# Performance work log

Hardware: AMD Instinct MI355X
Metric: run time of the kernel (lower is better)

The kernel has to match this reference:

```python
import jax, jax.numpy as jnp
import numpy as np

N_NODES = 100000
N_EDGES = 3200000
D_FEAT = 128
N1 = 128
N2 = 64
NUM_CLASSES = 10
NUM_GRAPHS = 256


def gcn_conv(x, edge_index, W, b, num_nodes):
    """PyG GCNConv: y = D^-1/2 (A+I) D^-1/2 (x W) + b, self-loops added."""
    src, dst = edge_index[0], edge_index[1]
    # degree including self-loop (edge weight 1)
    deg = jax.ops.segment_sum(jnp.ones_like(dst, dtype=x.dtype), dst,
                              num_segments=num_nodes) + 1.0
    dis = jnp.where(deg > 0, deg ** -0.5, 0.0)  # deg_inv_sqrt, [N]
    h = x @ W                                    # transform first, [N, out]
    norm = dis[src] * dis[dst]                   # [E]
    msg = h[src] * norm[:, None]                 # gather + scale, [E, out]
    agg = jax.ops.segment_sum(msg, dst, num_segments=num_nodes)
    agg = agg + h * (dis * dis)[:, None]         # self-loop contribution
    return agg + b


def global_mean_pool(x, batch, num_graphs):
    sums = jax.ops.segment_sum(x, batch, num_segments=num_graphs)
    cnt = jax.ops.segment_sum(jnp.ones((x.shape[0],), dtype=x.dtype), batch,
                              num_segments=num_graphs)
    return sums / jnp.maximum(cnt, 1.0)[:, None]


def setup_inputs() -> dict:
    key = jax.random.key(0)
    ks = jax.random.split(key, 8)
    x = jax.random.normal(ks[0], (N_NODES, D_FEAT), dtype=jnp.float32)
    edge_index = jax.random.randint(ks[1], (2, N_EDGES), 0, N_NODES, dtype=jnp.int64)
    batch = jnp.sort(jax.random.randint(ks[2], (N_NODES,), 0, NUM_GRAPHS, dtype=jnp.int64))
    W1 = jax.random.normal(ks[3], (D_FEAT, N1), dtype=jnp.float32) / np.sqrt(D_FEAT)
    b1 = jnp.zeros((N1,), dtype=jnp.float32)
    W2 = jax.random.normal(ks[4], (N1, N2), dtype=jnp.float32) / np.sqrt(N1)
    b2 = jnp.zeros((N2,), dtype=jnp.float32)
    Wfc = jax.random.normal(ks[5], (N2, NUM_CLASSES), dtype=jnp.float32) / np.sqrt(N2)
    bfc = jnp.zeros((NUM_CLASSES,), dtype=jnp.float32)
    return {"x": x, "edge_index": edge_index, "batch": batch,
            "W1": W1, "b1": b1, "W2": W2, "b2": b2,
            "Wfc": Wfc, "bfc": bfc, "num_graphs": NUM_GRAPHS}


def reference(x, edge_index, batch, W1, b1, W2, b2, Wfc, bfc, num_graphs):
    n = x.shape[0]
    h = gcn_conv(x, edge_index, W1, b1, n)
    h = jax.nn.relu(h)
    h = gcn_conv(h, edge_index, W2, b2, n)
    g = global_mean_pool(h, batch, num_graphs)   # [num_graphs, N2]
    # dropout is identity at inference
    return g @ Wfc + bfc                          # [num_graphs, num_classes]
```

## Files before the change

kernel.cpp:

```cpp
#include <hip/hip_runtime.h>
#include <math.h>

typedef unsigned int  u32;
typedef unsigned short u16;

#define TILE1 8192
#define BKW   256
#define CAP   9216

typedef __attribute__((ext_vector_type(8))) short bf16x8;
typedef __attribute__((ext_vector_type(4))) float f32x4;
typedef __attribute__((ext_vector_type(2))) float f32x2;
union frag_u { bf16x8 v; u32 u[4]; uint4 q; };

__device__ inline u32 bf16_rne(float f) {
    u32 u = __float_as_uint(f);
    return (u + 0x7FFFu + ((u >> 16) & 1u)) >> 16;
}
__device__ inline float bf_lo(u32 u) { return __uint_as_float(u << 16); }
__device__ inline float bf_hi(u32 u) { return __uint_as_float(u & 0xFFFF0000u); }

__device__ inline f32x2 up2(u32 u) {
    f32x2 t;
    t.x = __uint_as_float(u << 16);
    t.y = __uint_as_float(u & 0xFFFF0000u);
    return t;
}
__device__ inline void add8p(f32x2* a, uint4 q) {
    a[0] += up2(q.x); a[1] += up2(q.y); a[2] += up2(q.z); a[3] += up2(q.w);
}

__device__ inline u32 relu_pk(u32 v) {
    u32 s = v & 0x80008000u;
    u32 m = (s >> 15) * 0xFFFFu;
    return v & ~m;
}


__global__ __launch_bounds__(512) void k_part1(const int* __restrict__ ei,
                                               int* __restrict__ bucketCur,
                                               u32* __restrict__ tmp,
                                               int E, int N, int NBK) {
    __shared__ int hist[1024];
    __shared__ int base[512];
    const int tid = threadIdx.x;
    if (tid < NBK) { hist[tid] = 0; hist[512 + tid] = 0; }
    __syncthreads();

    const int rep = (tid & 1) << 9;
    const int t0 = blockIdx.x * TILE1;
    const int4* ei4s = (const int4*)ei;
    const int4* ei4d = (const int4*)(ei + E);
    const int q0 = t0 >> 2;
    const int QE = E >> 2;

    int sv[16], dv[16], key[16];
#pragma unroll
    for (int j = 0; j < 4; ++j) {
        int qi = q0 + j * 512 + tid;
        int4 s4 = make_int4(0, 0, 0, 0), d4 = make_int4(-1, -1, -1, -1);
        if (qi < QE) { s4 = ei4s[qi]; d4 = ei4d[qi]; }
        sv[4 * j + 0] = s4.x; dv[4 * j + 0] = d4.x;
        sv[4 * j + 1] = s4.y; dv[4 * j + 1] = d4.y;
        sv[4 * j + 2] = s4.z; dv[4 * j + 2] = d4.z;
        sv[4 * j + 3] = s4.w; dv[4 * j + 3] = d4.w;
    }
#pragma unroll
    for (int j = 0; j < 16; ++j) {
        key[j] = -1;
        if ((unsigned)dv[j] < (unsigned)N && (unsigned)sv[j] < (unsigned)N) {
            key[j] = dv[j] >> 8;
            atomicAdd(&hist[key[j] + rep], 1);
        }
    }
    __syncthreads();
    if (tid < NBK) {
        int tot = hist[tid] + hist[512 + tid];
        base[tid] = atomicAdd(&bucketCur[tid], tot);
        hist[tid] = 0;
    }
    __syncthreads();
#pragma unroll
    for (int j = 0; j < 16; ++j) {
        if (key[j] >= 0) {
            int slot = atomicAdd(&hist[key[j]], 1);
            int off = base[key[j]] + slot;
            if (off < CAP)
                tmp[(size_t)key[j] * CAP + off] =
                    ((u32)(dv[j] & 255) << 17) | (u32)sv[j];
        }
    }
}

__global__ __launch_bounds__(512) void k_part2(const int* __restrict__ bucketCnt,
                                               const u32* __restrict__ tmp,
                                               int* __restrict__ csr,
                                               int* __restrict__ rowptr,
                                               float* __restrict__ dis,
                                               int* __restrict__ gdegH,
                                               int N, int NBK) {
    __shared__ int hist[256];
    __shared__ int ts[512];
    __shared__ int degh[256];
    __shared__ int sStart;
    const int b = blockIdx.x;
    const int t = threadIdx.x;

    if (t < 256) degh[t] = 0;
    int myCnt = (t < NBK) ? bucketCnt[t] : 0;
    ts[t] = myCnt;
    __syncthreads();
    for (int off = 1; off < 512; off <<= 1) {
        int u = (t >= off) ? ts[t - off] : 0;
        __syncthreads();
        ts[t] += u;
        __syncthreads();
    }
    if (t == b) sStart = ts[t] - myCnt;
    if (b == 0 && t == NBK - 1) rowptr[N] = ts[t];
    __syncthreads();
    const int start = sStart;
    const int cnt = bucketCnt[b];
    const u32* src = tmp + (size_t)b * CAP;

    if (t < 256) hist[t] = 0;
    __syncthreads();
    for (int i = t; i < cnt; i += 512)
        atomicAdd(&hist[src[i] >> 17], 1);
    __syncthreads();

    int h = (t < 256) ? hist[t] : 0;
    ts[t] = h;
    __syncthreads();
    for (int off = 1; off < 512; off <<= 1) {
        int u = (t >= off) ? ts[t - off] : 0;
        __syncthreads();
        ts[t] += u;
        __syncthreads();
    }
    if (t < 256) hist[t] = ts[t] - h;
    __syncthreads();

    if (t < 256) {
        int gn = (b << 8) + t;
        if (gn < N) {
            int e0 = hist[t];
            int e1 = (t < 255) ? hist[t + 1] : cnt;
            rowptr[gn] = start + e0;
            int d = e1 - e0;
            dis[gn] = rsqrtf((float)d + 1.0f);
            atomicAdd(&degh[d < 255 ? d : 255], 1);
        }
    }
    __syncthreads();

    if (t < 256 && degh[t]) atomicAdd(&gdegH[t], degh[t]);

    for (int i = t; i < cnt; i += 512) {
        u32 v = src[i];
        int p = atomicAdd(&hist[v >> 17], 1);
        csr[start + p] = (int)(v & 0x1FFFFu);
    }
}


__global__ __launch_bounds__(256) void k_prefix(const int* __restrict__ gdegH,
                                                int* __restrict__ binBase) {
    __shared__ int ts[256];
    int t = threadIdx.x;
    int v = gdegH[t];
    ts[t] = v;
    __syncthreads();
    for (int off = 1; off < 256; off <<= 1) {
        int u = (t >= off) ? ts[t - off] : 0;
        __syncthreads();
        ts[t] += u;
        __syncthreads();
    }
    binBase[t] = ts[t] - v;
}

__global__ __launch_bounds__(512) void k_scatter(const int* __restrict__ rowptr,
                                                 int* __restrict__ binBase,
                                                 int* __restrict__ perm, int N) {
    __shared__ int lh[256];
    __shared__ int lb[256];
    int t = threadIdx.x;
    int i = blockIdx.x * 512 + t;
    if (t < 256) lh[t] = 0;
    __syncthreads();
    int d = 0, slot = 0;
    if (i < N) {
        d = rowptr[i + 1] - rowptr[i];
        if (d > 255) d = 255;
        slot = atomicAdd(&lh[d], 1);
    }
    __syncthreads();
    if (t < 256) lb[t] = lh[t] ? atomicAdd(&binBase[t], lh[t]) : 0;
    __syncthreads();
    if (i < N) perm[lb[d] + slot] = i;
}


__global__ __launch_bounds__(256) void k_convW(
    const float* __restrict__ W1, const float* __restrict__ W2,
    u32* __restrict__ W1h, u32* __restrict__ W1l,
    u32* __restrict__ W2h, u32* __restrict__ W2l,
    int* __restrict__ bucketCur, int* __restrict__ gdegH, int NBK)
{
    int idx = blockIdx.x * 256 + threadIdx.x;
    if (idx < NBK) bucketCur[idx] = 0;
    if (idx < 256) gdegH[idx] = 0;
    if (idx < 8192) {
        int n = idx >> 6, k = (idx & 63) * 2;
        float w0 = W1[k * 128 + n], w1 = W1[(k + 1) * 128 + n];
        u32 h0 = bf16_rne(w0), h1 = bf16_rne(w1);
        u32 l0 = bf16_rne(w0 - __uint_as_float(h0 << 16));
        u32 l1 = bf16_rne(w1 - __uint_as_float(h1 << 16));
        W1h[idx] = h0 | (h1 << 16);
        W1l[idx] = l0 | (l1 << 16);
    } else if (idx < 12288) {
        int i2 = idx - 8192;
        int n = i2 >> 6, k = (i2 & 63) * 2;
        float w0 = W2[k * 64 + n], w1 = W2[(k + 1) * 64 + n];
        u32 h0 = bf16_rne(w0), h1 = bf16_rne(w1);
        u32 l0 = bf16_rne(w0 - __uint_as_float(h0 << 16));
        u32 l1 = bf16_rne(w1 - __uint_as_float(h1 << 16));
        W2h[i2] = h0 | (h1 << 16);
        W2l[i2] = l0 | (l1 << 16);
    }
}


__global__ __launch_bounds__(256) void k_gemm1m(
    const float* __restrict__ X, const u32* __restrict__ Wh,
    const u32* __restrict__ Wl, const float* __restrict__ dis,
    u32* __restrict__ Hb, int M)
{
    __shared__ uint4 sW[4096];
    const int tid = threadIdx.x;
    const uint4* Wh4 = (const uint4*)Wh;
    const uint4* Wl4 = (const uint4*)Wl;
#pragma unroll
    for (int i = 0; i < 8; ++i) {
        int idx = tid + i * 256;
        int l = idx >> 4, j = idx & 15;
        int js = j ^ (l & 7);
        sW[l * 16 + js] = Wh4[idx];
        sW[2048 + l * 16 + js] = Wl4[idx];
    }
    __syncthreads();

    const int w = tid >> 6, lane = tid & 63;
    const int mrow = blockIdx.x * 64 + w * 16;
    const int m16 = lane & 15, quad = lane >> 4;
    int gm = mrow + m16; if (gm >= M) gm = M - 1;

    frag_u Ah[4], Al[4];
    const float* xr = X + (size_t)gm * 128;
#pragma unroll
    for (int kt = 0; kt < 4; ++kt) {
        int kb = kt * 32 + quad * 8;
        float4 xa = *(const float4*)(xr + kb);
        float4 xb = *(const float4*)(xr + kb + 4);
        float xe[8] = {xa.x, xa.y, xa.z, xa.w, xb.x, xb.y, xb.z, xb.w};
#pragma unroll
        for (int j = 0; j < 4; ++j) {
            u32 h0 = bf16_rne(xe[2 * j]),     h1 = bf16_rne(xe[2 * j + 1]);
            u32 l0 = bf16_rne(xe[2 * j]     - __uint_as_float(h0 << 16));
            u32 l1 = bf16_rne(xe[2 * j + 1] - __uint_as_float(h1 << 16));
            Ah[kt].u[j] = h0 | (h1 << 16);
            Al[kt].u[j] = l0 | (l1 << 16);
        }
    }

    float dv[4];
#pragma unroll
    for (int r = 0; r < 4; ++r) {
        int gR = mrow + quad * 4 + r;
        dv[r] = (gR < M) ? dis[gR] : 0.f;
    }

#pragma unroll
    for (int nt = 0; nt < 8; ++nt) {
        f32x4 acc = {0.f, 0.f, 0.f, 0.f};
        int l = nt * 16 + m16;
        int swz = l & 7;
#pragma unroll
        for (int kt = 0; kt < 4; ++kt) {
            frag_u Bh, Bl;
            int jb = (kt * 4 + quad) ^ swz;
            Bh.q = sW[l * 16 + jb];
            Bl.q = sW[2048 + l * 16 + jb];
            acc = __builtin_amdgcn_mfma_f32_16x16x32_bf16(Al[kt].v, Bh.v, acc, 0, 0, 0);
            acc = __builtin_amdgcn_mfma_f32_16x16x32_bf16(Ah[kt].v, Bl.v, acc, 0, 0, 0);
            acc = __builtin_amdgcn_mfma_f32_16x16x32_bf16(Ah[kt].v, Bh.v, acc, 0, 0, 0);
        }
#pragma unroll
        for (int r = 0; r < 4; ++r) {
            float vs = acc[r] * dv[r];
            float vo = __shfl_xor(vs, 1, 64);
            if ((m16 & 1) == 0) {
                int gR = mrow + quad * 4 + r;
                if (gR < M)
                    Hb[(size_t)gR * 64 + nt * 8 + (m16 >> 1)] =
                        bf16_rne(vs) | (bf16_rne(vo) << 16);
            }
        }
    }
}


__global__ __launch_bounds__(256) void k_gemm2m(
    const u32* __restrict__ Xb, const u32* __restrict__ Wh,
    const u32* __restrict__ Wl, const float* __restrict__ dis,
    u32* __restrict__ Hb, int M)
{
    __shared__ uint4 sW[2176];
    const int tid = threadIdx.x;
    const uint4* Wh4 = (const uint4*)Wh;
    const uint4* Wl4 = (const uint4*)Wl;
#pragma unroll
    for (int i = 0; i < 4; ++i) {
        int idx = tid + i * 256;
        int l = idx >> 4, j = idx & 15;
        sW[l * 17 + j] = Wh4[l * 16 + j];
        sW[1088 + l * 17 + j] = Wl4[l * 16 + j];
    }
    __syncthreads();

    const int w = tid >> 6, lane = tid & 63;
    const int mrow = blockIdx.x * 64 + w * 16;
    const int m16 = lane & 15, quad = lane >> 4;
    int gm = mrow + m16; if (gm >= M) gm = M - 1;

    const uint4* X4 = (const uint4*)Xb;
    frag_u A[4];
#pragma unroll
    for (int kt = 0; kt < 4; ++kt) {
        A[kt].q = X4[(size_t)gm * 16 + kt * 4 + quad];
#pragma unroll
        for (int j = 0; j < 4; ++j) A[kt].u[j] = relu_pk(A[kt].u[j]);
    }

    float dv[4];
#pragma unroll
    for (int r = 0; r < 4; ++r) {
        int gR = mrow + quad * 4 + r;
        dv[r] = (gR < M) ? dis[gR] : 0.f;
    }

#pragma unroll
    for (int nt = 0; nt < 4; ++nt) {
        f32x4 acc = {0.f, 0.f, 0.f, 0.f};
        int l = nt * 16 + m16;
#pragma unroll
        for (int kt = 0; kt < 4; ++kt) {
            frag_u Bh, Bl;
            Bh.q = sW[l * 17 + kt * 4 + quad];
            Bl.q = sW[1088 + l * 17 + kt * 4 + quad];
            acc = __builtin_amdgcn_mfma_f32_16x16x32_bf16(A[kt].v, Bl.v, acc, 0, 0, 0);
            acc = __builtin_amdgcn_mfma_f32_16x16x32_bf16(A[kt].v, Bh.v, acc, 0, 0, 0);
        }
#pragma unroll
        for (int r = 0; r < 4; ++r) {
            float vs = acc[r] * dv[r];
            float vo = __shfl_xor(vs, 1, 64);
            if ((m16 & 1) == 0) {
                int gR = mrow + quad * 4 + r;
                if (gR < M)
                    Hb[(size_t)gR * 32 + nt * 8 + (m16 >> 1)] =
                        bf16_rne(vs) | (bf16_rne(vo) << 16);
            }
        }
    }
}


template <int LGS>
__global__ __launch_bounds__(256) void k_aggs(
    const int* __restrict__ rowptr, const int* __restrict__ csr,
    const int* __restrict__ perm, const float* __restrict__ dis,
    const u32* __restrict__ Hb, const float* __restrict__ bias,
    u32* __restrict__ AGGb, int N)
{
    const int LG = 1 << LGS;
    const int SH = LGS + 4;
    int gid = blockIdx.x * 256 + threadIdx.x;
    int s = gid >> LGS;
    int li = threadIdx.x & (LG - 1);
    if (s >= N) return;
    int n = perm[s];
    int e = rowptr[n];
    int s1 = rowptr[n + 1];
    const float dn = dis[n];
    const char* hb = (const char*)Hb;
    const u32 off = (u32)li << 4;

    f32x2 acc[4];
#pragma unroll
    for (int j = 0; j < 4; ++j) acc[j] = 0.f;

    for (; e + 8 <= s1; e += 8) {
        u32 b0 = (u32)csr[e + 0] << SH;
        u32 b1 = (u32)csr[e + 1] << SH;
        u32 b2 = (u32)csr[e + 2] << SH;
        u32 b3 = (u32)csr[e + 3] << SH;
        u32 b4 = (u32)csr[e + 4] << SH;
        u32 b5 = (u32)csr[e + 5] << SH;
        u32 b6 = (u32)csr[e + 6] << SH;
        u32 b7 = (u32)csr[e + 7] << SH;
        uint4 q0 = *(const uint4*)(hb + b0 + off);
        uint4 q1 = *(const uint4*)(hb + b1 + off);
        uint4 q2 = *(const uint4*)(hb + b2 + off);
        uint4 q3 = *(const uint4*)(hb + b3 + off);
        uint4 q4 = *(const uint4*)(hb + b4 + off);
        uint4 q5 = *(const uint4*)(hb + b5 + off);
        uint4 q6 = *(const uint4*)(hb + b6 + off);
        uint4 q7 = *(const uint4*)(hb + b7 + off);
        add8p(acc, q0); add8p(acc, q1); add8p(acc, q2); add8p(acc, q3);
        add8p(acc, q4); add8p(acc, q5); add8p(acc, q6); add8p(acc, q7);
    }
    for (; e + 2 <= s1; e += 2) {
        u32 b0 = (u32)csr[e + 0] << SH;
        u32 b1 = (u32)csr[e + 1] << SH;
        uint4 q0 = *(const uint4*)(hb + b0 + off);
        uint4 q1 = *(const uint4*)(hb + b1 + off);
        add8p(acc, q0); add8p(acc, q1);
    }
    if (e < s1) {
        u32 b0 = (u32)csr[e] << SH;
        uint4 q0 = *(const uint4*)(hb + b0 + off);
        add8p(acc, q0);
    }
    {
        uint4 q = *(const uint4*)(hb + ((u32)n << SH) + off);
        add8p(acc, q);
    }

    float4 b0 = ((const float4*)bias)[li * 2 + 0];
    float4 b1 = ((const float4*)bias)[li * 2 + 1];
    uint4 p;
    p.x = bf16_rne(fmaf(dn, acc[0].x, b0.x)) | (bf16_rne(fmaf(dn, acc[0].y, b0.y)) << 16);
    p.y = bf16_rne(fmaf(dn, acc[1].x, b0.z)) | (bf16_rne(fmaf(dn, acc[1].y, b0.w)) << 16);
    p.z = bf16_rne(fmaf(dn, acc[2].x, b1.x)) | (bf16_rne(fmaf(dn, acc[2].y, b1.y)) << 16);
    p.w = bf16_rne(fmaf(dn, acc[3].x, b1.z)) | (bf16_rne(fmaf(dn, acc[3].y, b1.w)) << 16);
    ((uint4*)AGGb)[(size_t)n * LG + li] = p;
}


__device__ inline int lower_bound(const int* __restrict__ b, int n, int v) {
    int lo = 0, hi = n;
    while (lo < hi) { int m = (lo + hi) >> 1; if (b[m] < v) lo = m + 1; else hi = m; }
    return lo;
}

__global__ __launch_bounds__(256) void k_poolfc(
    const int* __restrict__ batch, const u32* __restrict__ AGGb2,
    const float* __restrict__ Wfc, const float* __restrict__ bfc,
    float* __restrict__ out, int n)
{
    int g = blockIdx.x;
    int start = lower_bound(batch, n, g);
    int end   = lower_bound(batch, n, g + 1);
    int tid = threadIdx.x;
    int f = tid & 63, stripe = tid >> 6;
    int ui = f >> 1, hi = f & 1;
    float acc = 0.f;
    for (int i = start + stripe; i < end; i += 4) {
        u32 v = AGGb2[(size_t)i * 32 + ui];
        acc += hi ? bf_hi(v) : bf_lo(v);
    }
    __shared__ float red[256];
    __shared__ float mean[64];
    red[tid] = acc;
    __syncthreads();
    if (tid < 64) {
        float s = red[tid] + red[tid + 64] + red[tid + 128] + red[tid + 192];
        float c = (float)(end - start);
        mean[tid] = s / fmaxf(c, 1.0f);
    }
    __syncthreads();
    if (tid < 10) {
        float o = bfc[tid];
        for (int k = 0; k < 64; ++k)
            o = fmaf(mean[k], Wfc[k * 10 + tid], o);
        out[g * 10 + tid] = o;
    }
}


extern "C" void kernel_launch(void* const* d_in, const int* in_sizes, int n_in,
                              void* d_out, int out_size, void* d_ws, size_t ws_size,
                              hipStream_t stream)
{
    const float* x    = (const float*)d_in[0];
    const int*   ei   = (const int*)d_in[1];
    const int*   batch= (const int*)d_in[2];
    const float* W1   = (const float*)d_in[3];
    const float* b1   = (const float*)d_in[4];
    const float* W2   = (const float*)d_in[5];
    const float* b2   = (const float*)d_in[6];
    const float* Wfc  = (const float*)d_in[7];
    const float* bfc  = (const float*)d_in[8];
    float* out = (float*)d_out;

    const int N  = in_sizes[0] / 128;
    const int E  = in_sizes[1] / 2;
    const int ng = out_size / 10;

    const int NBK = (N + BKW - 1) / BKW;

    int*   rowptr    = (int*)d_ws;
    int*   bucketCur = rowptr + 102400;
    float* dis       = (float*)(bucketCur + 512);
    int*   csr       = (int*)(dis + 102400);
    u32*   tmp       = (u32*)(csr + E);
    u32*   Hb1       = tmp;
    u32*   agg2b     = tmp;
    u32*   agg1b     = (u32*)((int*)tmp + (size_t)N * 64);
    u16*   Hb2       = (u16*)((int*)agg1b + (size_t)N * 128);
    u32*   W1h       = (u32*)((int*)Hb2 + (size_t)N * 32);
    u32*   W1l       = W1h + 8192;
    u32*   W2h       = W1l + 8192;
    u32*   W2l       = W2h + 4096;
    int*   perm      = (int*)(W2l + 4096);
    int*   gdegH     = perm + N;
    int*   binBase   = gdegH + 256;

    k_convW<<<48, 256, 0, stream>>>(W1, W2, W1h, W1l, W2h, W2l, bucketCur, gdegH, NBK);
    k_part1<<<(E + TILE1 - 1) / TILE1, 512, 0, stream>>>(ei, bucketCur, tmp, E, N, NBK);
    k_part2<<<NBK, 512, 0, stream>>>(bucketCur, tmp, csr, rowptr, dis, gdegH, N, NBK);
    k_prefix<<<1, 256, 0, stream>>>(gdegH, binBase);
    k_scatter<<<(N + 511) / 512, 512, 0, stream>>>(rowptr, binBase, perm, N);

    k_gemm1m<<<(N + 63) / 64, 256, 0, stream>>>(x, W1h, W1l, dis, Hb1, N);
    k_aggs<4><<<(N * 16 + 255) / 256, 256, 0, stream>>>(rowptr, csr, perm, dis, Hb1, b1, agg1b, N);

    k_gemm2m<<<(N + 63) / 64, 256, 0, stream>>>(agg1b, W2h, W2l, dis, (u32*)Hb2, N);
    k_aggs<3><<<(N * 8 + 255) / 256, 256, 0, stream>>>(rowptr, csr, perm, dis, (const u32*)Hb2, b2, agg2b, N);

    k_poolfc<<<ng, 256, 0, stream>>>(batch, agg2b, Wfc, bfc, out, N);
}
```

Measured before the change: 404.4 us.

## Drop degree-sorted permutation, split layer-1 aggregation into column halves, widen GEMM tiles

Removes the degree histogram, prefix and scatter kernels that built a degree-sorted node permutation, so the aggregation now walks nodes in natural order. The 128-wide layer-1 aggregation runs as two passes over 64-column halves, each with 8 lanes per node, which shrinks the gathered working set per pass and may improve cache hit rates at the cost of reading the CSR twice. Both GEMM kernels now compute 32 rows per wave (128 per block), reusing each B fragment loaded from shared memory across two MFMA tiles. The risks are load imbalance without degree sorting and higher register pressure in the GEMMs.

```diff
diff --git a/kernel.cpp b/kernel.cpp
--- a/kernel.cpp
+++ b/kernel.cpp
@@ -97,16 +97,13 @@
                                                int* __restrict__ csr,
                                                int* __restrict__ rowptr,
                                                float* __restrict__ dis,
-                                               int* __restrict__ gdegH,
                                                int N, int NBK) {
     __shared__ int hist[256];
     __shared__ int ts[512];
-    __shared__ int degh[256];
     __shared__ int sStart;
     const int b = blockIdx.x;
     const int t = threadIdx.x;
 
-    if (t < 256) degh[t] = 0;
     int myCnt = (t < NBK) ? bucketCnt[t] : 0;
     ts[t] = myCnt;
     __syncthreads();
@@ -147,14 +144,10 @@
             int e0 = hist[t];
             int e1 = (t < 255) ? hist[t + 1] : cnt;
             rowptr[gn] = start + e0;
-            int d = e1 - e0;
-            dis[gn] = rsqrtf((float)d + 1.0f);
-            atomicAdd(&degh[d < 255 ? d : 255], 1);
-        }
-    }
-    __syncthreads();
-
-    if (t < 256 && degh[t]) atomicAdd(&gdegH[t], degh[t]);
+            dis[gn] = rsqrtf((float)(e1 - e0) + 1.0f);
+        }
+    }
+    __syncthreads();
 
     for (int i = t; i < cnt; i += 512) {
         u32 v = src[i];
@@ -164,53 +157,14 @@
 }
 
 
-__global__ __launch_bounds__(256) void k_prefix(const int* __restrict__ gdegH,
-                                                int* __restrict__ binBase) {
-    __shared__ int ts[256];
-    int t = threadIdx.x;
-    int v = gdegH[t];
-    ts[t] = v;
-    __syncthreads();
-    for (int off = 1; off < 256; off <<= 1) {
-        int u = (t >= off) ? ts[t - off] : 0;
-        __syncthreads();
-        ts[t] += u;
-        __syncthreads();
-    }
-    binBase[t] = ts[t] - v;
-}
-
-__global__ __launch_bounds__(512) void k_scatter(const int* __restrict__ rowptr,
-                                                 int* __restrict__ binBase,
-                                                 int* __restrict__ perm, int N) {
-    __shared__ int lh[256];
-    __shared__ int lb[256];
-    int t = threadIdx.x;
-    int i = blockIdx.x * 512 + t;
-    if (t < 256) lh[t] = 0;
-    __syncthreads();
-    int d = 0, slot = 0;
-    if (i < N) {
-        d = rowptr[i + 1] - rowptr[i];
-        if (d > 255) d = 255;
-        slot = atomicAdd(&lh[d], 1);
-    }
-    __syncthreads();
-    if (t < 256) lb[t] = lh[t] ? atomicAdd(&binBase[t], lh[t]) : 0;
-    __syncthreads();
-    if (i < N) perm[lb[d] + slot] = i;
-}
-
-
 __global__ __launch_bounds__(256) void k_convW(
     const float* __restrict__ W1, const float* __restrict__ W2,
     u32* __restrict__ W1h, u32* __restrict__ W1l,
     u32* __restrict__ W2h, u32* __restrict__ W2l,
-    int* __restrict__ bucketCur, int* __restrict__ gdegH, int NBK)
+    int* __restrict__ bucketCur, int NBK)
 {
     int idx = blockIdx.x * 256 + threadIdx.x;
     if (idx < NBK) bucketCur[idx] = 0;
-    if (idx < 256) gdegH[idx] = 0;
     if (idx < 8192) {
         int n = idx >> 6, k = (idx & 63) * 2;
         float w0 = W1[k * 128 + n], w1 = W1[(k + 1) * 128 + n];
@@ -252,38 +206,44 @@
     __syncthreads();
 
     const int w = tid >> 6, lane = tid & 63;
-    const int mrow = blockIdx.x * 64 + w * 16;
+    const int mrow = blockIdx.x * 128 + w * 32;
     const int m16 = lane & 15, quad = lane >> 4;
-    int gm = mrow + m16; if (gm >= M) gm = M - 1;
-
-    frag_u Ah[4], Al[4];
-    const float* xr = X + (size_t)gm * 128;
-#pragma unroll
-    for (int kt = 0; kt < 4; ++kt) {
-        int kb = kt * 32 + quad * 8;
-        float4 xa = *(const float4*)(xr + kb);
-        float4 xb = *(const float4*)(xr + kb + 4);
-        float xe[8] = {xa.x, xa.y, xa.z, xa.w, xb.x, xb.y, xb.z, xb.w};
-#pragma unroll
-        for (int j = 0; j < 4; ++j) {
-            u32 h0 = bf16_rne(xe[2 * j]),     h1 = bf16_rne(xe[2 * j + 1]);
-            u32 l0 = bf16_rne(xe[2 * j]     - __uint_as_float(h0 << 16));
-            u32 l1 = bf16_rne(xe[2 * j + 1] - __uint_as_float(h1 << 16));
-            Ah[kt].u[j] = h0 | (h1 << 16);
-            Al[kt].u[j] = l0 | (l1 << 16);
-        }
-    }
-
-    float dv[4];
-#pragma unroll
-    for (int r = 0; r < 4; ++r) {
-        int gR = mrow + quad * 4 + r;
-        dv[r] = (gR < M) ? dis[gR] : 0.f;
-    }
+
+    frag_u Ah[2][4], Al[2][4];
+#pragma unroll
+    for (int t = 0; t < 2; ++t) {
+        int gm = mrow + t * 16 + m16; if (gm >= M) gm = M - 1;
+        const float* xr = X + (size_t)gm * 128;
+#pragma unroll
+        for (int kt = 0; kt < 4; ++kt) {
+            int kb = kt * 32 + quad * 8;
+            float4 xa = *(const float4*)(xr + kb);
+            float4 xb = *(const float4*)(xr + kb + 4);
+            float xe[8] = {xa.x, xa.y, xa.z, xa.w, xb.x, xb.y, xb.z, xb.w};
+#pragma unroll
+            for (int j = 0; j < 4; ++j) {
+                u32 h0 = bf16_rne(xe[2 * j]),     h1 = bf16_rne(xe[2 * j + 1]);
+                u32 l0 = bf16_rne(xe[2 * j]     - __uint_as_float(h0 << 16));
+                u32 l1 = bf16_rne(xe[2 * j + 1] - __uint_as_float(h1 << 16));
+                Ah[t][kt].u[j] = h0 | (h1 << 16);
+                Al[t][kt].u[j] = l0 | (l1 << 16);
+            }
+        }
+    }
+
+    float dv[2][4];
+#pragma unroll
+    for (int t = 0; t < 2; ++t)
+#pragma unroll
+        for (int r = 0; r < 4; ++r) {
+            int gR = mrow + t * 16 + quad * 4 + r;
+            dv[t][r] = (gR < M) ? dis[gR] : 0.f;
+        }
 
 #pragma unroll
     for (int nt = 0; nt < 8; ++nt) {
-        f32x4 acc = {0.f, 0.f, 0.f, 0.f};
+        f32x4 acc0 = {0.f, 0.f, 0.f, 0.f};
+        f32x4 acc1 = {0.f, 0.f, 0.f, 0.f};
         int l = nt * 16 + m16;
         int swz = l & 7;
 #pragma unroll
@@ -292,19 +252,28 @@
             int jb = (kt * 4 + quad) ^ swz;
             Bh.q = sW[l * 16 + jb];
             Bl.q = sW[2048 + l * 16 + jb];
-            acc = __builtin_amdgcn_mfma_f32_16x16x32_bf16(Al[kt].v, Bh.v, acc, 0, 0, 0);
-            acc = __builtin_amdgcn_mfma_f32_16x16x32_bf16(Ah[kt].v, Bl.v, acc, 0, 0, 0);
-            acc = __builtin_amdgcn_mfma_f32_16x16x32_bf16(Ah[kt].v, Bh.v, acc, 0, 0, 0);
+            acc0 = __builtin_amdgcn_mfma_f32_16x16x32_bf16(Al[0][kt].v, Bh.v, acc0, 0, 0, 0);
+            acc0 = __builtin_amdgcn_mfma_f32_16x16x32_bf16(Ah[0][kt].v, Bl.v, acc0, 0, 0, 0);
+            acc0 = __builtin_amdgcn_mfma_f32_16x16x32_bf16(Ah[0][kt].v, Bh.v, acc0, 0, 0, 0);
+            acc1 = __builtin_amdgcn_mfma_f32_16x16x32_bf16(Al[1][kt].v, Bh.v, acc1, 0, 0, 0);
+            acc1 = __builtin_amdgcn_mfma_f32_16x16x32_bf16(Ah[1][kt].v, Bl.v, acc1, 0, 0, 0);
+            acc1 = __builtin_amdgcn_mfma_f32_16x16x32_bf16(Ah[1][kt].v, Bh.v, acc1, 0, 0, 0);
         }
 #pragma unroll
         for (int r = 0; r < 4; ++r) {
-            float vs = acc[r] * dv[r];
-            float vo = __shfl_xor(vs, 1, 64);
+            float vs0 = acc0[r] * dv[0][r];
+            float vo0 = __shfl_xor(vs0, 1, 64);
+            float vs1 = acc1[r] * dv[1][r];
+            float vo1 = __shfl_xor(vs1, 1, 64);
             if ((m16 & 1) == 0) {
-                int gR = mrow + quad * 4 + r;
-                if (gR < M)
-                    Hb[(size_t)gR * 64 + nt * 8 + (m16 >> 1)] =
-                        bf16_rne(vs) | (bf16_rne(vo) << 16);
+                int gR0 = mrow + quad * 4 + r;
+                if (gR0 < M)
+                    Hb[(size_t)gR0 * 64 + nt * 8 + (m16 >> 1)] =
+                        bf16_rne(vs0) | (bf16_rne(vo0) << 16);
+                int gR1 = mrow + 16 + quad * 4 + r;
+                if (gR1 < M)
+                    Hb[(size_t)gR1 * 64 + nt * 8 + (m16 >> 1)] =
+                        bf16_rne(vs1) | (bf16_rne(vo1) << 16);
             }
         }
     }
@@ -330,72 +299,82 @@
     __syncthreads();
 
     const int w = tid >> 6, lane = tid & 63;
-    const int mrow = blockIdx.x * 64 + w * 16;
+    const int mrow = blockIdx.x * 128 + w * 32;
     const int m16 = lane & 15, quad = lane >> 4;
-    int gm = mrow + m16; if (gm >= M) gm = M - 1;
 
     const uint4* X4 = (const uint4*)Xb;
-    frag_u A[4];
-#pragma unroll
-    for (int kt = 0; kt < 4; ++kt) {
-        A[kt].q = X4[(size_t)gm * 16 + kt * 4 + quad];
-#pragma unroll
-        for (int j = 0; j < 4; ++j) A[kt].u[j] = relu_pk(A[kt].u[j]);
-    }
-
-    float dv[4];
-#pragma unroll
-    for (int r = 0; r < 4; ++r) {
-        int gR = mrow + quad * 4 + r;
-        dv[r] = (gR < M) ? dis[gR] : 0.f;
-    }
+    frag_u A[2][4];
+#pragma unroll
+    for (int t = 0; t < 2; ++t) {
+        int gm = mrow + t * 16 + m16; if (gm >= M) gm = M - 1;
+#pragma unroll
+        for (int kt = 0; kt < 4; ++kt) {
+            A[t][kt].q = X4[(size_t)gm * 16 + kt * 4 + quad];
+#pragma unroll
+            for (int j = 0; j < 4; ++j) A[t][kt].u[j] = relu_pk(A[t][kt].u[j]);
+        }
+    }
+
+    float dv[2][4];
+#pragma unroll
+    for (int t = 0; t < 2; ++t)
+#pragma unroll
+        for (int r = 0; r < 4; ++r) {
+            int gR = mrow + t * 16 + quad * 4 + r;
+            dv[t][r] = (gR < M) ? dis[gR] : 0.f;
+        }
 
 #pragma unroll
     for (int nt = 0; nt < 4; ++nt) {
-        f32x4 acc = {0.f, 0.f, 0.f, 0.f};
+        f32x4 acc0 = {0.f, 0.f, 0.f, 0.f};
+        f32x4 acc1 = {0.f, 0.f, 0.f, 0.f};
         int l = nt * 16 + m16;
 #pragma unroll
         for (int kt = 0; kt < 4; ++kt) {
             frag_u Bh, Bl;
             Bh.q = sW[l * 17 + kt * 4 + quad];
             Bl.q = sW[1088 + l * 17 + kt * 4 + quad];
-            acc = __builtin_amdgcn_mfma_f32_16x16x32_bf16(A[kt].v, Bl.v, acc, 0, 0, 0);
-            acc = __builtin_amdgcn_mfma_f32_16x16x32_bf16(A[kt].v, Bh.v, acc, 0, 0, 0);
+            acc0 = __builtin_amdgcn_mfma_f32_16x16x32_bf16(A[0][kt].v, Bl.v, acc0, 0, 0, 0);
+            acc0 = __builtin_amdgcn_mfma_f32_16x16x32_bf16(A[0][kt].v, Bh.v, acc0, 0, 0, 0);
+            acc1 = __builtin_amdgcn_mfma_f32_16x16x32_bf16(A[1][kt].v, Bl.v, acc1, 0, 0, 0);
+            acc1 = __builtin_amdgcn_mfma_f32_16x16x32_bf16(A[1][kt].v, Bh.v, acc1, 0, 0, 0);
         }
 #pragma unroll
         for (int r = 0; r < 4; ++r) {
-            float vs = acc[r] * dv[r];
-            float vo = __shfl_xor(vs, 1, 64);
+            float vs0 = acc0[r] * dv[0][r];
+            float vo0 = __shfl_xor(vs0, 1, 64);
+            float vs1 = acc1[r] * dv[1][r];
+            float vo1 = __shfl_xor(vs1, 1, 64);
             if ((m16 & 1) == 0) {
-                int gR = mrow + quad * 4 + r;
-                if (gR < M)
-                    Hb[(size_t)gR * 32 + nt * 8 + (m16 >> 1)] =
-                        bf16_rne(vs) | (bf16_rne(vo) << 16);
+                int gR0 = mrow + quad * 4 + r;
+                if (gR0 < M)
+                    Hb[(size_t)gR0 * 32 + nt * 8 + (m16 >> 1)] =
+                        bf16_rne(vs0) | (bf16_rne(vo0) << 16);
+                int gR1 = mrow + 16 + quad * 4 + r;
+                if (gR1 < M)
+                    Hb[(size_t)gR1 * 32 + nt * 8 + (m16 >> 1)] =
+                        bf16_rne(vs1) | (bf16_rne(vo1) << 16);
             }
         }
     }
 }
 
 
-template <int LGS>
-__global__ __launch_bounds__(256) void k_aggs(
+template <int SH, int POFF>
+__global__ __launch_bounds__(256) void k_aggh(
     const int* __restrict__ rowptr, const int* __restrict__ csr,
-    const int* __restrict__ perm, const float* __restrict__ dis,
-    const u32* __restrict__ Hb, const float* __restrict__ bias,
-    u32* __restrict__ AGGb, int N)
+    const float* __restrict__ dis, const u32* __restrict__ Hb,
+    const float* __restrict__ bias, u32* __restrict__ AGGb, int N)
 {
-    const int LG = 1 << LGS;
-    const int SH = LGS + 4;
     int gid = blockIdx.x * 256 + threadIdx.x;
-    int s = gid >> LGS;
-    int li = threadIdx.x & (LG - 1);
-    if (s >= N) return;
-    int n = perm[s];
+    int n = gid >> 3;
+    int li = threadIdx.x & 7;
+    if (n >= N) return;
     int e = rowptr[n];
     int s1 = rowptr[n + 1];
     const float dn = dis[n];
     const char* hb = (const char*)Hb;
-    const u32 off = (u32)li << 4;
+    const u32 off = (u32)(POFF + li * 16);
 
     f32x2 acc[4];
 #pragma unroll
@@ -438,14 +417,14 @@
         add8p(acc, q);
     }
 
-    float4 b0 = ((const float4*)bias)[li * 2 + 0];
-    float4 b1 = ((const float4*)bias)[li * 2 + 1];
+    float4 b0 = ((const float4*)bias)[POFF / 8 + li * 2 + 0];
+    float4 b1 = ((const float4*)bias)[POFF / 8 + li * 2 + 1];
     uint4 p;
     p.x = bf16_rne(fmaf(dn, acc[0].x, b0.x)) | (bf16_rne(fmaf(dn, acc[0].y, b0.y)) << 16);
     p.y = bf16_rne(fmaf(dn, acc[1].x, b0.z)) | (bf16_rne(fmaf(dn, acc[1].y, b0.w)) << 16);
     p.z = bf16_rne(fmaf(dn, acc[2].x, b1.x)) | (bf16_rne(fmaf(dn, acc[2].y, b1.y)) << 16);
     p.w = bf16_rne(fmaf(dn, acc[3].x, b1.z)) | (bf16_rne(fmaf(dn, acc[3].y, b1.w)) << 16);
-    ((uint4*)AGGb)[(size_t)n * LG + li] = p;
+    ((uint4*)AGGb)[(size_t)n * (1 << (SH - 4)) + POFF / 16 + li] = p;
 }
 
 
@@ -524,21 +503,17 @@
     u32*   W1l       = W1h + 8192;
     u32*   W2h       = W1l + 8192;
     u32*   W2l       = W2h + 4096;
-    int*   perm      = (int*)(W2l + 4096);
-    int*   gdegH     = perm + N;
-    int*   binBase   = gdegH + 256;
-
-    k_convW<<<48, 256, 0, stream>>>(W1, W2, W1h, W1l, W2h, W2l, bucketCur, gdegH, NBK);
+
+    k_convW<<<48, 256, 0, stream>>>(W1, W2, W1h, W1l, W2h, W2l, bucketCur, NBK);
     k_part1<<<(E + TILE1 - 1) / TILE1, 512, 0, stream>>>(ei, bucketCur, tmp, E, N, NBK);
-    k_part2<<<NBK, 512, 0, stream>>>(bucketCur, tmp, csr, rowptr, dis, gdegH, N, NBK);
-    k_prefix<<<1, 256, 0, stream>>>(gdegH, binBase);
-    k_scatter<<<(N + 511) / 512, 512, 0, stream>>>(rowptr, binBase, perm, N);
-
-    k_gemm1m<<<(N + 63) / 64, 256, 0, stream>>>(x, W1h, W1l, dis, Hb1, N);
-    k_aggs<4><<<(N * 16 + 255) / 256, 256, 0, stream>>>(rowptr, csr, perm, dis, Hb1, b1, agg1b, N);
-
-    k_gemm2m<<<(N + 63) / 64, 256, 0, stream>>>(agg1b, W2h, W2l, dis, (u32*)Hb2, N);
-    k_aggs<3><<<(N * 8 + 255) / 256, 256, 0, stream>>>(rowptr, csr, perm, dis, (const u32*)Hb2, b2, agg2b, N);
+    k_part2<<<NBK, 512, 0, stream>>>(bucketCur, tmp, csr, rowptr, dis, N, NBK);
+
+    k_gemm1m<<<(N + 127) / 128, 256, 0, stream>>>(x, W1h, W1l, dis, Hb1, N);
+    k_aggh<8, 0><<<(N * 8 + 255) / 256, 256, 0, stream>>>(rowptr, csr, dis, Hb1, b1, agg1b, N);
+    k_aggh<8, 128><<<(N * 8 + 255) / 256, 256, 0, stream>>>(rowptr, csr, dis, Hb1, b1, agg1b, N);
+
+    k_gemm2m<<<(N + 127) / 128, 256, 0, stream>>>(agg1b, W2h, W2l, dis, (u32*)Hb2, N);
+    k_aggh<7, 0><<<(N * 8 + 255) / 256, 256, 0, stream>>>(rowptr, csr, dis, (const u32*)Hb2, b2, agg2b, N);
 
     k_poolfc<<<ng, 256, 0, stream>>>(batch, agg2b, Wfc, bfc, out, N);
 }
```

Result: faster. 384.3 us (-5.0%).
